# Kernel tuning notes

Hardware: AMD Instinct MI355X
Metric: run time of the kernel (lower is better)

Reference implementation:

```python
import jax, jax.numpy as jnp
import numpy as np

HIDDEN = 128
EDGE = 64
EPS = 1e-5

def setup_inputs() -> dict:
    key = jax.random.key(0)
    ks = jax.random.split(key, 12)
    B, N, D = 8, 256, HIDDEN
    h = jax.random.normal(ks[0], (B, N, D), dtype=jnp.float32)
    edge_feats = jax.random.normal(ks[1], (B, N, N, 3), dtype=jnp.float32)
    adj_mask = jax.random.bernoulli(ks[2], 0.5, (B, N, N))
    s = lambda fan_in: 1.0 / np.sqrt(fan_in)
    W1 = jax.random.uniform(ks[3], (D + 3, EDGE), minval=-s(D + 3), maxval=s(D + 3))
    b1 = jnp.zeros((EDGE,), jnp.float32)
    W2 = jax.random.uniform(ks[4], (EDGE, D), minval=-s(EDGE), maxval=s(EDGE))
    b2 = jnp.zeros((D,), jnp.float32)
    U1 = jax.random.uniform(ks[5], (3 * D, D), minval=-s(3 * D), maxval=s(3 * D))
    b3 = jnp.zeros((D,), jnp.float32)
    U2 = jax.random.uniform(ks[6], (D, D), minval=-s(D), maxval=s(D))
    b4 = jnp.zeros((D,), jnp.float32)
    gamma = jnp.ones((D,), jnp.float32)
    beta = jnp.zeros((D,), jnp.float32)
    return {"h": h, "edge_feats": edge_feats, "adj_mask": adj_mask,
            "W1": W1, "b1": b1, "W2": W2, "b2": b2,
            "U1": U1, "b3": b3, "U2": U2, "b4": b4,
            "gamma": gamma, "beta": beta}

def reference(h, edge_feats, adj_mask, W1, b1, W2, b2, U1, b3, U2, b4, gamma, beta):
    B, N, D = h.shape
    # NOTE: torch does h.unsqueeze(2).expand(B,N,N,D): h_j[b,i,j,:] = h[b,i,:]
    h_j = jnp.broadcast_to(h[:, :, None, :], (B, N, N, D))
    gate_in = jnp.concatenate([h_j, edge_feats], axis=-1)          # (B,N,N,D+3)
    gates = jax.nn.sigmoid(jax.nn.relu(gate_in @ W1 + b1) @ W2 + b2)  # (B,N,N,D)
    mask_f = adj_mask.astype(h.dtype)[..., None]                    # (B,N,N,1)
    messages = gates * h_j * mask_f
    neighbor_count = jnp.clip(jnp.sum(mask_f, axis=2), 1.0)         # (B,N,1)
    agg_mean = jnp.sum(messages, axis=2) / neighbor_count           # (B,N,D)
    msgs_max = jnp.where(adj_mask[..., None], messages, -jnp.inf)
    agg_max = jnp.max(msgs_max, axis=2)
    agg_max = jnp.where(jnp.isinf(agg_max), 0.0, agg_max)
    upd_in = jnp.concatenate([h, agg_mean, agg_max], axis=-1)       # (B,N,3D)
    upd = jax.nn.relu(upd_in @ U1 + b3) @ U2 + b4
    x = h + upd
    mu = jnp.mean(x, axis=-1, keepdims=True)
    var = jnp.var(x, axis=-1, keepdims=True)
    return (x - mu) * jax.lax.rsqrt(var + EPS) * gamma + beta
```

## Files before the change

kernel.cpp:

```cpp
#include <hip/hip_runtime.h>
#include <hip/hip_bf16.h>
#include <math.h>

#define NN 256
#define DD 128
#define EE 64
#define APAD 392
#define RPAD 136

typedef __attribute__((ext_vector_type(8))) short short8;
typedef __attribute__((ext_vector_type(4))) float f32x4;

static __device__ __forceinline__ unsigned short f2bf(float f) {
    __hip_bfloat16 b = __float2bfloat16(f);
    return *reinterpret_cast<unsigned short*>(&b);
}

static __device__ __forceinline__ float sigm(float l) {
    return __fdividef(1.f, 1.f + __expf(-l));
}

static __device__ __forceinline__ short8 ldb(const float* __restrict__ B, int kbase, int d) {
    unsigned short tmp[8];
    #pragma unroll
    for (int j = 0; j < 8; ++j) tmp[j] = f2bf(B[(kbase + j) * DD + d]);
    return *(const short8*)tmp;
}

__global__ __launch_bounds__(256, 4)
void ecgc_gate(const float* __restrict__ h_g,
               const float* __restrict__ ef_g,
               const int*   __restrict__ mask_g,
               const float* __restrict__ W1_g,
               const float* __restrict__ b1_g,
               const float* __restrict__ W2_g,
               const float* __restrict__ b2_g,
               const float* __restrict__ U1_g,
               const float* __restrict__ U2_g,
               float*          __restrict__ aggf,
               unsigned short* __restrict__ u1t,
               unsigned short* __restrict__ u2t)
{
    const int bi   = blockIdx.x;
    const int t    = threadIdx.x;
    const int lane = t & 63;
    const int w    = t >> 6;
    const int m16  = lane & 15;
    const int quad = lane >> 4;
    const int bj   = t & 15;
    const int beb  = (t >> 4) << 2;

    __shared__ __align__(16) float sh_ef4[NN * 4];
    __shared__ __align__(16) float sh_q4[EE * 4];
    __shared__ float sh_basep[4 * EE];
    __shared__ float sh_w1e[3 * EE];
    __shared__ int   sh_jlist[NN], sh_wcnt[4], sh_cnt;
    __shared__ __align__(16) unsigned short sh_P[4][16 * EE];

    if (t < 32) {
        const int flat = bi * 32 + t;
        if (flat < 384 * DD) {
            const int d = flat / 384, k = flat - d * 384;
            u1t[((k >> 3) * DD + d) * 8 + (k & 7)] = f2bf(U1_g[k * DD + d]);
        } else {
            const int f2i = flat - 384 * DD;
            const int d = f2i >> 7, k = f2i & 127;
            u2t[((k >> 3) * DD + d) * 8 + (k & 7)] = f2bf(U2_g[k * DD + d]);
        }
    }

    {
        const float* efr = ef_g + (size_t)bi * NN * 3;
        sh_ef4[t * 4 + 0] = efr[t * 3 + 0];
        sh_ef4[t * 4 + 1] = efr[t * 3 + 1];
        sh_ef4[t * 4 + 2] = efr[t * 3 + 2];
        sh_ef4[t * 4 + 3] = 0.f;
    }
    if (t < 192) sh_w1e[t] = W1_g[(DD + (t >> 6)) * EE + (t & 63)];

    const int mk = (mask_g[bi * NN + t] != 0) ? 1 : 0;
    const unsigned long long bal = __ballot(mk);
    if (lane == 0) sh_wcnt[w] = __popcll(bal);
    const int pre = __popcll(bal & ((1ull << lane) - 1ull));

    {
        const int e = t & 63;
        float acc = 0.f;
        #pragma unroll 8
        for (int d = w * 32; d < w * 32 + 32; ++d)
            acc = fmaf(h_g[bi * DD + d], W1_g[d * EE + e], acc);
        sh_basep[w * EE + e] = acc;
    }

    const int dstripe = w * 32;
    short8 bfrag[2][2];
    float  nb2[2], hd2[2], flip[2];
    #pragma unroll
    for (int dt = 0; dt < 2; ++dt) {
        const int d = dstripe + 16 * dt + m16;
        nb2[dt] = b2_g[d];
        hd2[dt] = h_g[bi * DD + d];
        flip[dt] = (hd2[dt] >= 0.f) ? 1.f : -1.f;
        #pragma unroll
        for (int kh = 0; kh < 2; ++kh)
            bfrag[dt][kh] = ldb(W2_g, kh * 32 + quad * 8, d);
    }
    __syncthreads();

    {
        int wbase = 0;
        for (int ww = 0; ww < w; ++ww) wbase += sh_wcnt[ww];
        if (mk) sh_jlist[wbase + pre] = t;
        if (t == 0) sh_cnt = sh_wcnt[0] + sh_wcnt[1] + sh_wcnt[2] + sh_wcnt[3];
    }
    if (t < EE) {
        const float base = b1_g[t] + sh_basep[t] + sh_basep[EE + t] +
                           sh_basep[2 * EE + t] + sh_basep[3 * EE + t];
        sh_q4[t * 4 + 0] = base;
        sh_q4[t * 4 + 1] = sh_w1e[t];
        sh_q4[t * 4 + 2] = sh_w1e[EE + t];
        sh_q4[t * 4 + 3] = sh_w1e[2 * EE + t];
    }
    __syncthreads();

    f32x4 qreg[4];
    #pragma unroll
    for (int i = 0; i < 4; ++i) qreg[i] = *(const f32x4*)&sh_q4[(beb + i) * 4];

    const int cnt = sh_cnt;
    const int njt = (cnt + 15) >> 4;

    const int   sw_r = (m16 & 7) << 4;
    const char* prow = (const char*)&sh_P[0][m16 * EE];
    const int   offA = (quad * 16) ^ sw_r;
    const int   offB = (64 + quad * 16) ^ sw_r;
    char* pwr;
    {
        const int cb = 2 * beb;
        const int cs = (cb & 8) | ((((cb >> 4) ^ (bj & 7)) & 7) << 4);
        pwr = (char*)&sh_P[0][bj * EE] + cs;
    }

    float sum2[2] = {0.f, 0.f};
    float mm[2]   = {-3.0e38f, -3.0e38f};

    auto buildP = [&](int jtile, int bufbyte) {
        const int row = jtile * 16 + bj;
        int jl = sh_jlist[row];
        jl = (row < cnt) ? jl : 0;
        const float4 efv = *(const float4*)&sh_ef4[jl * 4];
        float v[4];
        #pragma unroll
        for (int i = 0; i < 4; ++i)
            v[i] = fmaxf(fmaf(efv.z, qreg[i][3], fmaf(efv.y, qreg[i][2],
                         fmaf(efv.x, qreg[i][1], qreg[i][0]))), 0.f);
        union { __hip_bfloat162 h2; unsigned int u; } a0, a1;
        a0.h2 = __float22bfloat162_rn(make_float2(v[0], v[1]));
        a1.h2 = __float22bfloat162_rn(make_float2(v[2], v[3]));
        *reinterpret_cast<uint2*>(pwr + bufbyte) = make_uint2(a0.u, a1.u);
    };

    if (njt > 0) buildP(0, 0);
    if (njt > 1) buildP(1, 2048);
    __syncthreads();

    for (int jt = 0; jt < njt; ++jt) {
        const int bo = (jt & 3) << 11;
        const short8 ua = *(const short8*)(prow + bo + offA);
        const short8 ub = *(const short8*)(prow + bo + offB);

        if (jt + 2 < njt) buildP(jt + 2, ((jt + 2) & 3) << 11);

        const bool tail = (jt == njt - 1) && (cnt & 15);
        #pragma unroll
        for (int dt = 0; dt < 2; ++dt) {
            f32x4 acc = {nb2[dt], nb2[dt], nb2[dt], nb2[dt]};
            acc = __builtin_amdgcn_mfma_f32_16x16x32_bf16(ua, bfrag[dt][0], acc, 0, 0, 0);
            acc = __builtin_amdgcn_mfma_f32_16x16x32_bf16(ub, bfrag[dt][1], acc, 0, 0, 0);
            if (!tail) {
                #pragma unroll
                for (int r = 0; r < 4; ++r) {
                    const float l = acc[r];
                    mm[dt] = fmaxf(mm[dt], l * flip[dt]);
                    sum2[dt] += sigm(l);
                }
            } else {
                #pragma unroll
                for (int r = 0; r < 4; ++r) {
                    const bool v = (jt * 16 + quad * 4 + r) < cnt;
                    const float lx = v ? acc[r] : -3.0e38f;
                    const float pf = v ? acc[r] * flip[dt] : -3.0e38f;
                    mm[dt] = fmaxf(mm[dt], pf);
                    sum2[dt] += sigm(lx);
                }
            }
        }
        if (jt & 1) __syncthreads();
    }

    #pragma unroll
    for (int dt = 0; dt < 2; ++dt) {
        float s = sum2[dt], M = mm[dt];
        s += __shfl_xor(s, 16, 64);  s += __shfl_xor(s, 32, 64);
        M  = fmaxf(M,  __shfl_xor(M, 16, 64));  M  = fmaxf(M,  __shfl_xor(M, 32, 64));
        if (quad == 0) {
            const int d = dstripe + 16 * dt + m16;
            const float hd = hd2[dt];
            float mean = 0.f, amax = 0.f;
            if (cnt > 0) {
                mean = hd * s * __fdividef(1.f, (float)cnt);
                amax = hd * sigm(flip[dt] * M);
            }
            aggf[bi * 256 + d]       = mean;
            aggf[bi * 256 + 128 + d] = amax;
        }
    }
}

__global__ __launch_bounds__(256, 2)
void ecgc_upd(const float* __restrict__ h_g,
              const float* __restrict__ aggf,
              const unsigned short* __restrict__ u1t,
              const unsigned short* __restrict__ u2t,
              const float* __restrict__ b3_g,
              const float* __restrict__ b4_g,
              const float* __restrict__ gam_g,
              const float* __restrict__ bet_g,
              float*       __restrict__ out_g)
{
    const int bi0  = blockIdx.x * 8;
    const int t    = threadIdx.x;
    const int lane = t & 63;
    const int w    = t >> 6;
    const int m16  = lane & 15;
    const int quad = lane >> 4;

    __shared__ __align__(16) unsigned short shA[16 * APAD];
    __shared__ __align__(16) unsigned short rbuf[16 * RPAD];
    __shared__ float sh_s[4 * 16], sh_s2[4 * 16], sh_mu[16], sh_rs[16];

    {
        const int row = t >> 4, q = t & 15;
        const int pr  = bi0 + (row & 7);
        const float* hrow = h_g  + (size_t)pr * DD;
        const float* wrow = aggf + (size_t)pr * 256;
        unsigned short tmp[24];
        #pragma unroll
        for (int c = 0; c < 24; ++c) {
            const int col = q * 24 + c;
            float v;
            if (col < 128)      v = hrow[col];
            else if (col < 256) v = wrow[col - 128];
            else                v = wrow[col - 256 + 128];
            tmp[c] = f2bf(v);
        }
        #pragma unroll
        for (int s8 = 0; s8 < 3; ++s8)
            *(short8*)&shA[row * APAD + q * 24 + s8 * 8] = *(const short8*)&tmp[s8 * 8];
    }
    __syncthreads();

    const int dstripe = w * 32;

    f32x4 acc[2];
    #pragma unroll
    for (int dt = 0; dt < 2; ++dt) {
        const float bb = b3_g[dstripe + dt * 16 + m16];
        acc[dt] = (f32x4){bb, bb, bb, bb};
    }
    for (int kk = 0; kk < 12; ++kk) {
        const short8 a0 = *(const short8*)&shA[m16 * APAD + kk * 32 + quad * 8];
        #pragma unroll
        for (int dt = 0; dt < 2; ++dt) {
            const int d = dstripe + dt * 16 + m16;
            const short8 b = *(const short8*)&u1t[(size_t)((kk * 4 + quad) * DD + d) * 8];
            acc[dt] = __builtin_amdgcn_mfma_f32_16x16x32_bf16(a0, b, acc[dt], 0, 0, 0);
        }
    }

    #pragma unroll
    for (int dt = 0; dt < 2; ++dt) {
        const int d = dstripe + dt * 16 + m16;
        #pragma unroll
        for (int r = 0; r < 4; ++r) {
            const int ro = quad * 4 + r;
            rbuf[ro * RPAD + d] = f2bf(fmaxf(acc[dt][r], 0.f));
        }
    }
    __syncthreads();

    f32x4 acc2[2];
    #pragma unroll
    for (int dt = 0; dt < 2; ++dt) {
        const float bb = b4_g[dstripe + dt * 16 + m16];
        acc2[dt] = (f32x4){bb, bb, bb, bb};
    }
    for (int kk = 0; kk < 4; ++kk) {
        const short8 a0 = *(const short8*)&rbuf[m16 * RPAD + kk * 32 + quad * 8];
        #pragma unroll
        for (int dt = 0; dt < 2; ++dt) {
            const int d = dstripe + dt * 16 + m16;
            const short8 b = *(const short8*)&u2t[(size_t)((kk * 4 + quad) * DD + d) * 8];
            acc2[dt] = __builtin_amdgcn_mfma_f32_16x16x32_bf16(a0, b, acc2[dt], 0, 0, 0);
        }
    }

    float xv[2][4];
    #pragma unroll
    for (int dt = 0; dt < 2; ++dt) {
        const int d = dstripe + dt * 16 + m16;
        #pragma unroll
        for (int r = 0; r < 4; ++r) {
            const int ro = quad * 4 + r;
            xv[dt][r] = h_g[(size_t)(bi0 + (ro & 7)) * DD + d] + acc2[dt][r];
        }
    }

    #pragma unroll
    for (int r = 0; r < 4; ++r) {
        float s  = xv[0][r] + xv[1][r];
        float s2 = xv[0][r] * xv[0][r] + xv[1][r] * xv[1][r];
        #pragma unroll
        for (int off = 1; off < 16; off <<= 1) {
            s  += __shfl_xor(s,  off, 64);
            s2 += __shfl_xor(s2, off, 64);
        }
        if (m16 == 0) {
            const int ro = quad * 4 + r;
            sh_s[w * 16 + ro]  = s;
            sh_s2[w * 16 + ro] = s2;
        }
    }
    __syncthreads();
    if (t < 16) {
        const float S  = sh_s[t]  + sh_s[16 + t]  + sh_s[32 + t]  + sh_s[48 + t];
        const float S2 = sh_s2[t] + sh_s2[16 + t] + sh_s2[32 + t] + sh_s2[48 + t];
        const float mu  = S * (1.f / 128.f);
        const float var = S2 * (1.f / 128.f) - mu * mu;
        sh_mu[t] = mu;
        sh_rs[t] = rsqrtf(var + 1e-5f);
    }
    __syncthreads();

    #pragma unroll
    for (int dt = 0; dt < 2; ++dt) {
        const int d = dstripe + dt * 16 + m16;
        const float ga = gam_g[d], be = bet_g[d];
        #pragma unroll
        for (int r = 0; r < 4; ++r) {
            const int ro = quad * 4 + r;
            if (ro < 8)
                out_g[(size_t)(bi0 + ro) * DD + d] =
                    (xv[dt][r] - sh_mu[ro]) * sh_rs[ro] * ga + be;
        }
    }
}

extern "C" void kernel_launch(void* const* d_in, const int* in_sizes, int n_in,
                              void* d_out, int out_size, void* d_ws, size_t ws_size,
                              hipStream_t stream) {
    float* aggf = (float*)d_ws;
    unsigned short* u1t = (unsigned short*)((char*)d_ws + (size_t)2048 * 256 * 4);
    unsigned short* u2t = u1t + 384 * DD;
    ecgc_gate<<<8 * NN, 256, 0, stream>>>(
        (const float*)d_in[0],
        (const float*)d_in[1],
        (const int*)d_in[2],
        (const float*)d_in[3],
        (const float*)d_in[4],
        (const float*)d_in[5],
        (const float*)d_in[6],
        (const float*)d_in[7],
        (const float*)d_in[9],
        aggf, u1t, u2t);
    ecgc_upd<<<NN, 256, 0, stream>>>(
        (const float*)d_in[0],
        aggf, u1t, u2t,
        (const float*)d_in[8],
        (const float*)d_in[10],
        (const float*)d_in[11],
        (const float*)d_in[12],
        (float*)d_out);
}
```

Measured before the change: 118.2 us.

## Fuse update MLP and layernorm into gate kernel, dropping second launch

Removes the separate update kernel and the workspace round-trip. Each gate block now keeps its row's h, mean and max aggregates in shared memory and runs the U1/U2 matvecs in fp32 FMA with float4 reads of U1/U2 straight from global, then does the layernorm in the same block. This drops the bf16 weight pre-transpose, the aggregate write/read and a kernel launch. In exchange, every one of 2048 blocks re-reads the full U1 and U2 weights (largely L2 hits) and uses scalar FMA instead of MFMA, which adds per-block tail latency.

Measured after the change: 118.3 us, median of 2. No clear change (+0.0%).

```diff
diff --git a/kernel.cpp b/kernel.cpp
--- a/kernel.cpp
+++ b/kernel.cpp
@@ -5,8 +5,6 @@
 #define NN 256
 #define DD 128
 #define EE 64
-#define APAD 392
-#define RPAD 136
 
 typedef __attribute__((ext_vector_type(8))) short short8;
 typedef __attribute__((ext_vector_type(4))) float f32x4;
@@ -28,18 +26,20 @@
 }
 
 __global__ __launch_bounds__(256, 4)
-void ecgc_gate(const float* __restrict__ h_g,
-               const float* __restrict__ ef_g,
-               const int*   __restrict__ mask_g,
-               const float* __restrict__ W1_g,
-               const float* __restrict__ b1_g,
-               const float* __restrict__ W2_g,
-               const float* __restrict__ b2_g,
-               const float* __restrict__ U1_g,
-               const float* __restrict__ U2_g,
-               float*          __restrict__ aggf,
-               unsigned short* __restrict__ u1t,
-               unsigned short* __restrict__ u2t)
+void ecgc_fused(const float* __restrict__ h_g,
+                const float* __restrict__ ef_g,
+                const int*   __restrict__ mask_g,
+                const float* __restrict__ W1_g,
+                const float* __restrict__ b1_g,
+                const float* __restrict__ W2_g,
+                const float* __restrict__ b2_g,
+                const float* __restrict__ U1_g,
+                const float* __restrict__ b3_g,
+                const float* __restrict__ U2_g,
+                const float* __restrict__ b4_g,
+                const float* __restrict__ gam_g,
+                const float* __restrict__ bet_g,
+                float*       __restrict__ out_g)
 {
     const int bi   = blockIdx.x;
     const int t    = threadIdx.x;
@@ -56,19 +56,11 @@
     __shared__ float sh_w1e[3 * EE];
     __shared__ int   sh_jlist[NN], sh_wcnt[4], sh_cnt;
     __shared__ __align__(16) unsigned short sh_P[4][16 * EE];
-
-    if (t < 32) {
-        const int flat = bi * 32 + t;
-        if (flat < 384 * DD) {
-            const int d = flat / 384, k = flat - d * 384;
-            u1t[((k >> 3) * DD + d) * 8 + (k & 7)] = f2bf(U1_g[k * DD + d]);
-        } else {
-            const int f2i = flat - 384 * DD;
-            const int d = f2i >> 7, k = f2i & 127;
-            u2t[((k >> 3) * DD + d) * 8 + (k & 7)] = f2bf(U2_g[k * DD + d]);
-        }
-    }
-
+    __shared__ __align__(16) float sh_x[384];
+    __shared__ float sh_y[DD];
+    __shared__ float sh_red[4];
+
+    if (t < DD) sh_x[t] = h_g[bi * DD + t];
     {
         const float* efr = ef_g + (size_t)bi * NN * 3;
         sh_ef4[t * 4 + 0] = efr[t * 3 + 0];
@@ -211,158 +203,78 @@
                 mean = hd * s * __fdividef(1.f, (float)cnt);
                 amax = hd * sigm(flip[dt] * M);
             }
-            aggf[bi * 256 + d]       = mean;
-            aggf[bi * 256 + 128 + d] = amax;
-        }
-    }
-}
-
-__global__ __launch_bounds__(256, 2)
-void ecgc_upd(const float* __restrict__ h_g,
-              const float* __restrict__ aggf,
-              const unsigned short* __restrict__ u1t,
-              const unsigned short* __restrict__ u2t,
-              const float* __restrict__ b3_g,
-              const float* __restrict__ b4_g,
-              const float* __restrict__ gam_g,
-              const float* __restrict__ bet_g,
-              float*       __restrict__ out_g)
-{
-    const int bi0  = blockIdx.x * 8;
-    const int t    = threadIdx.x;
-    const int lane = t & 63;
-    const int w    = t >> 6;
-    const int m16  = lane & 15;
-    const int quad = lane >> 4;
-
-    __shared__ __align__(16) unsigned short shA[16 * APAD];
-    __shared__ __align__(16) unsigned short rbuf[16 * RPAD];
-    __shared__ float sh_s[4 * 16], sh_s2[4 * 16], sh_mu[16], sh_rs[16];
-
-    {
-        const int row = t >> 4, q = t & 15;
-        const int pr  = bi0 + (row & 7);
-        const float* hrow = h_g  + (size_t)pr * DD;
-        const float* wrow = aggf + (size_t)pr * 256;
-        unsigned short tmp[24];
-        #pragma unroll
-        for (int c = 0; c < 24; ++c) {
-            const int col = q * 24 + c;
-            float v;
-            if (col < 128)      v = hrow[col];
-            else if (col < 256) v = wrow[col - 128];
-            else                v = wrow[col - 256 + 128];
-            tmp[c] = f2bf(v);
-        }
-        #pragma unroll
-        for (int s8 = 0; s8 < 3; ++s8)
-            *(short8*)&shA[row * APAD + q * 24 + s8 * 8] = *(const short8*)&tmp[s8 * 8];
-    }
-    __syncthreads();
-
-    const int dstripe = w * 32;
-
-    f32x4 acc[2];
-    #pragma unroll
-    for (int dt = 0; dt < 2; ++dt) {
-        const float bb = b3_g[dstripe + dt * 16 + m16];
-        acc[dt] = (f32x4){bb, bb, bb, bb};
-    }
-    for (int kk = 0; kk < 12; ++kk) {
-        const short8 a0 = *(const short8*)&shA[m16 * APAD + kk * 32 + quad * 8];
-        #pragma unroll
-        for (int dt = 0; dt < 2; ++dt) {
-            const int d = dstripe + dt * 16 + m16;
-            const short8 b = *(const short8*)&u1t[(size_t)((kk * 4 + quad) * DD + d) * 8];
-            acc[dt] = __builtin_amdgcn_mfma_f32_16x16x32_bf16(a0, b, acc[dt], 0, 0, 0);
-        }
-    }
-
-    #pragma unroll
-    for (int dt = 0; dt < 2; ++dt) {
-        const int d = dstripe + dt * 16 + m16;
-        #pragma unroll
-        for (int r = 0; r < 4; ++r) {
-            const int ro = quad * 4 + r;
-            rbuf[ro * RPAD + d] = f2bf(fmaxf(acc[dt][r], 0.f));
-        }
-    }
-    __syncthreads();
-
-    f32x4 acc2[2];
-    #pragma unroll
-    for (int dt = 0; dt < 2; ++dt) {
-        const float bb = b4_g[dstripe + dt * 16 + m16];
-        acc2[dt] = (f32x4){bb, bb, bb, bb};
-    }
-    for (int kk = 0; kk < 4; ++kk) {
-        const short8 a0 = *(const short8*)&rbuf[m16 * RPAD + kk * 32 + quad * 8];
-        #pragma unroll
-        for (int dt = 0; dt < 2; ++dt) {
-            const int d = dstripe + dt * 16 + m16;
-            const short8 b = *(const short8*)&u2t[(size_t)((kk * 4 + quad) * DD + d) * 8];
-            acc2[dt] = __builtin_amdgcn_mfma_f32_16x16x32_bf16(a0, b, acc2[dt], 0, 0, 0);
-        }
-    }
-
-    float xv[2][4];
-    #pragma unroll
-    for (int dt = 0; dt < 2; ++dt) {
-        const int d = dstripe + dt * 16 + m16;
-        #pragma unroll
-        for (int r = 0; r < 4; ++r) {
-            const int ro = quad * 4 + r;
-            xv[dt][r] = h_g[(size_t)(bi0 + (ro & 7)) * DD + d] + acc2[dt][r];
-        }
-    }
-
-    #pragma unroll
-    for (int r = 0; r < 4; ++r) {
-        float s  = xv[0][r] + xv[1][r];
-        float s2 = xv[0][r] * xv[0][r] + xv[1][r] * xv[1][r];
-        #pragma unroll
-        for (int off = 1; off < 16; off <<= 1) {
-            s  += __shfl_xor(s,  off, 64);
-            s2 += __shfl_xor(s2, off, 64);
-        }
-        if (m16 == 0) {
-            const int ro = quad * 4 + r;
-            sh_s[w * 16 + ro]  = s;
-            sh_s2[w * 16 + ro] = s2;
-        }
-    }
-    __syncthreads();
-    if (t < 16) {
-        const float S  = sh_s[t]  + sh_s[16 + t]  + sh_s[32 + t]  + sh_s[48 + t];
-        const float S2 = sh_s2[t] + sh_s2[16 + t] + sh_s2[32 + t] + sh_s2[48 + t];
+            sh_x[128 + d] = mean;
+            sh_x[256 + d] = amax;
+        }
+    }
+    __syncthreads();
+
+    float* sh_p = sh_ef4;
+
+    {
+        const int e4 = (t & 31) * 4;
+        const int ks = (t >> 5) * 48;
+        f32x4 a = {0.f, 0.f, 0.f, 0.f};
+        for (int kk = 0; kk < 48; ++kk) {
+            const float  xk = sh_x[ks + kk];
+            const float4 u  = *(const float4*)&U1_g[(size_t)(ks + kk) * DD + e4];
+            a[0] = fmaf(xk, u.x, a[0]); a[1] = fmaf(xk, u.y, a[1]);
+            a[2] = fmaf(xk, u.z, a[2]); a[3] = fmaf(xk, u.w, a[3]);
+        }
+        *(f32x4*)&sh_p[(t >> 5) * DD + e4] = a;
+    }
+    __syncthreads();
+    if (t < DD) {
+        float y = b3_g[t];
+        #pragma unroll
+        for (int s = 0; s < 8; ++s) y += sh_p[s * DD + t];
+        sh_y[t] = fmaxf(y, 0.f);
+    }
+    __syncthreads();
+
+    {
+        const int d4 = (t & 31) * 4;
+        const int es = (t >> 5) * 16;
+        f32x4 a = {0.f, 0.f, 0.f, 0.f};
+        for (int ee = 0; ee < 16; ++ee) {
+            const float  ye = sh_y[es + ee];
+            const float4 u  = *(const float4*)&U2_g[(size_t)(es + ee) * DD + d4];
+            a[0] = fmaf(ye, u.x, a[0]); a[1] = fmaf(ye, u.y, a[1]);
+            a[2] = fmaf(ye, u.z, a[2]); a[3] = fmaf(ye, u.w, a[3]);
+        }
+        *(f32x4*)&sh_p[(t >> 5) * DD + d4] = a;
+    }
+    __syncthreads();
+
+    float xv = 0.f;
+    if (t < DD) {
+        xv = sh_x[t] + b4_g[t];
+        #pragma unroll
+        for (int s = 0; s < 8; ++s) xv += sh_p[s * DD + t];
+        float s1 = xv, s2v = xv * xv;
+        #pragma unroll
+        for (int off = 1; off < 64; off <<= 1) {
+            s1  += __shfl_xor(s1,  off, 64);
+            s2v += __shfl_xor(s2v, off, 64);
+        }
+        if (lane == 0) { sh_red[2 * w] = s1; sh_red[2 * w + 1] = s2v; }
+    }
+    __syncthreads();
+    if (t < DD) {
+        const float S   = sh_red[0] + sh_red[2];
+        const float S2  = sh_red[1] + sh_red[3];
         const float mu  = S * (1.f / 128.f);
         const float var = S2 * (1.f / 128.f) - mu * mu;
-        sh_mu[t] = mu;
-        sh_rs[t] = rsqrtf(var + 1e-5f);
-    }
-    __syncthreads();
-
-    #pragma unroll
-    for (int dt = 0; dt < 2; ++dt) {
-        const int d = dstripe + dt * 16 + m16;
-        const float ga = gam_g[d], be = bet_g[d];
-        #pragma unroll
-        for (int r = 0; r < 4; ++r) {
-            const int ro = quad * 4 + r;
-            if (ro < 8)
-                out_g[(size_t)(bi0 + ro) * DD + d] =
-                    (xv[dt][r] - sh_mu[ro]) * sh_rs[ro] * ga + be;
-        }
+        const float rs  = rsqrtf(var + 1e-5f);
+        out_g[(size_t)bi * DD + t] = (xv - mu) * rs * gam_g[t] + bet_g[t];
     }
 }
 
 extern "C" void kernel_launch(void* const* d_in, const int* in_sizes, int n_in,
                               void* d_out, int out_size, void* d_ws, size_t ws_size,
                               hipStream_t stream) {
-    float* aggf = (float*)d_ws;
-    unsigned short* u1t = (unsigned short*)((char*)d_ws + (size_t)2048 * 256 * 4);
-    unsigned short* u2t = u1t + 384 * DD;
-    ecgc_gate<<<8 * NN, 256, 0, stream>>>(
+    (void)d_ws; (void)ws_size;
+    ecgc_fused<<<8 * NN, 256, 0, stream>>>(
         (const float*)d_in[0],
         (const float*)d_in[1],
         (const int*)d_in[2],
@@ -371,12 +283,8 @@
         (const float*)d_in[5],
         (const float*)d_in[6],
         (const float*)d_in[7],
+        (const float*)d_in[8],
         (const float*)d_in[9],
-        aggf, u1t, u2t);
-    ecgc_upd<<<NN, 256, 0, stream>>>(
-        (const float*)d_in[0],
-        aggf, u1t, u2t,
-        (const float*)d_in[8],
         (const float*)d_in[10],
         (const float*)d_in[11],
         (const float*)d_in[12],
```
